# Performance work log

Hardware: AMD Instinct MI355X
Metric: run time of the kernel (lower is better)

Reference implementation:

```python
import jax, jax.numpy as jnp
import numpy as np

B, Q, K, D, H = 4, 2048, 2048, 512, 8
HD = D // H
_INF = -1e30


def setup_inputs() -> dict:
    key = jax.random.key(0)
    ks = jax.random.split(key, 8)
    scale = 1.0 / HD ** 0.5
    return {
        "query": jax.random.normal(ks[0], (B, Q, D), jnp.float32),
        "key": jax.random.normal(ks[1], (B, K, D), jnp.float32),
        "value": jax.random.normal(ks[2], (B, K, D), jnp.float32),
        "Wq": jax.random.normal(ks[3], (D, D), jnp.float32) * scale,  # [out,in]
        "Wk": jax.random.normal(ks[4], (D, D), jnp.float32) * scale,
        "Wv": jax.random.normal(ks[5], (D, D), jnp.float32) * scale,
        "Wo": jax.random.normal(ks[6], (D, D), jnp.float32) * scale,
        "attn_mask": jax.random.randint(ks[7], (B, K), 0, 2, jnp.int32),
    }


def reference(query, key, value, Wq, Wk, Wv, Wo, attn_mask):
    bsz, qlen, _ = query.shape
    klen = key.shape[1]
    head_q = (query @ Wq.T).reshape(bsz, qlen, H, HD)
    head_k = (key @ Wk.T).reshape(bsz, klen, H, HD)
    head_v = (value @ Wv.T).reshape(bsz, klen, H, HD)
    scale = 1.0 / HD ** 0.5
    # [b, i, j, n] score tensor, as in the torch einsum 'bind,bjnd->bijn'
    attn_score = jnp.einsum('bind,bjnd->bijn', head_q, head_k) * scale
    mask = (attn_mask == 0)[:, None, :, None]  # dim-2 mask branch
    attn_score = jnp.where(mask, _INF, attn_score)
    attn_prob = jax.nn.softmax(attn_score, axis=2)  # softmax over key axis j
    attn_vec = jnp.einsum('bijn,bjnd->bind', attn_prob, head_v)
    attn_vec = attn_vec.reshape(bsz, qlen, H * HD)
    return attn_vec @ Wo.T
```

## Files before the change

### kernel.cpp

```cpp
#include <hip/hip_runtime.h>

constexpr int Bc   = 4;
constexpr int Qlen = 2048;
constexpr int Klen = 2048;
constexpr int Dm   = 512;
constexpr int Hh   = 8;
constexpr int HDim = 64;

typedef __attribute__((ext_vector_type(8))) short short8;
typedef __attribute__((ext_vector_type(8))) _Float16 half8;
typedef __attribute__((ext_vector_type(2))) __fp16 fp16x2;
typedef __attribute__((ext_vector_type(4))) float f32x4;

__device__ __forceinline__ f32x4 MFMA16(short8 a, short8 b, f32x4 c) {
  return __builtin_amdgcn_mfma_f32_16x16x32_f16(
      __builtin_bit_cast(half8, a), __builtin_bit_cast(half8, b), c, 0, 0, 0);
}

__device__ __forceinline__ void gload_lds16(const void* g, void* l) {
  __builtin_amdgcn_global_load_lds(
      (const __attribute__((address_space(1))) void*)g,
      (__attribute__((address_space(3))) void*)l, 16, 0, 0);
}

__device__ __forceinline__ unsigned short f2h(float f) {
  _Float16 h = (_Float16)f;
  return __builtin_bit_cast(unsigned short, h);
}

__device__ __forceinline__ unsigned pk2h(float a, float b) {
  fp16x2 h = __builtin_amdgcn_cvt_pkrtz(a, b);
  return __builtin_bit_cast(unsigned, h);
}

__global__ __launch_bounds__(256) void cvt4(
    const float* __restrict__ s0, const float* __restrict__ s1,
    const float* __restrict__ s2, const float* __restrict__ s3,
    unsigned short* __restrict__ o0, unsigned short* __restrict__ o1,
    unsigned short* __restrict__ o2, unsigned short* __restrict__ o3,
    const int* __restrict__ msk, float* __restrict__ biasf) {
  const int seg = blockIdx.y;
  int i = (blockIdx.x * 256 + threadIdx.x) * 4;
  if (seg < 4) {
    const float* s = (seg == 0) ? s0 : (seg == 1) ? s1 : (seg == 2) ? s2 : s3;
    unsigned short* o = (seg == 0) ? o0 : (seg == 1) ? o1 : (seg == 2) ? o2 : o3;
    float4 x = *(const float4*)(s + i);
    unsigned t[2] = {pk2h(x.x, x.y), pk2h(x.z, x.w)};
    *(uint2*)(o + i) = *(const uint2*)t;
  } else if (i + 3 < Bc * Klen) {
    int4 m = *(const int4*)(msk + i);
    float4 bo;
    bo.x = (m.x == 0) ? -60000.0f : 0.0f;
    bo.y = (m.y == 0) ? -60000.0f : 0.0f;
    bo.z = (m.z == 0) ? -60000.0f : 0.0f;
    bo.w = (m.w == 0) ? -60000.0f : 0.0f;
    *(float4*)(biasf + i) = bo;
  }
}

__global__ __launch_bounds__(256) void cvt_in(
    const float* __restrict__ q, const float* __restrict__ k,
    const float* __restrict__ v,
    unsigned short* __restrict__ qh, unsigned short* __restrict__ kh,
    unsigned short* __restrict__ vh) {
  const int seg = blockIdx.y;
  const float* s = (seg == 0) ? q : (seg == 1) ? k : v;
  unsigned short* o = (seg == 0) ? qh : (seg == 1) ? kh : vh;
  int i = (blockIdx.x * 256 + threadIdx.x) * 4;
  float4 x = *(const float4*)(s + i);
  unsigned t[2] = {pk2h(x.x, x.y), pk2h(x.z, x.w)};
  *(uint2*)(o + i) = *(const uint2*)t;
}

template <bool F16A>
__global__ __launch_bounds__(256) void gemm_qkv(
    const float* __restrict__ q_in,
    const float* __restrict__ k_in,
    const float* __restrict__ v_in,
    const unsigned short* __restrict__ qh,
    const unsigned short* __restrict__ kh,
    const unsigned short* __restrict__ vh,
    const unsigned short* __restrict__ Wqh,
    const unsigned short* __restrict__ Wkh,
    const unsigned short* __restrict__ Wvh,
    unsigned short* __restrict__ Qp,
    unsigned short* __restrict__ Kp,
    unsigned short* __restrict__ Vp) {
  __shared__ unsigned short As[128 * 32];
  __shared__ unsigned short Bs[128 * 32];
  const int tid = threadIdx.x;
  const int w = tid >> 6, l = tid & 63;
  const int quad = l >> 4, l15 = l & 15;
  const int m0 = blockIdx.x * 128;
  const int n0 = blockIdx.y * 128;
  const int seg = n0 >> 9;
  const int f0  = n0 & 511;
  const float* Af = (seg == 0) ? q_in : (seg == 1) ? k_in : v_in;
  const unsigned short* Ah = (seg == 0) ? qh : (seg == 1) ? kh : vh;
  const unsigned short* W = (seg == 0) ? Wqh : (seg == 1) ? Wkh : Wvh;
  unsigned short* dst = (seg == 0) ? Qp : (seg == 1) ? Kp : Vp;

  f32x4 acc[4][4] = {};
  const int lrow = l >> 2;
  const int lcol = (l & 3) * 8;
  const int wm = (w >> 1) * 64, wn = (w & 1) * 64;

  for (int kk = 0; kk < 512; kk += 32) {
#pragma unroll
    for (int i = 0; i < 2; ++i) {
      int row = w * 32 + i * 16 + lrow;
      if constexpr (F16A) {
        gload_lds16(Ah + (size_t)(m0 + row) * 512 + kk + lcol, &As[row * 32 + lcol]);
      } else {
        const float* ap = Af + (size_t)(m0 + row) * 512 + kk + lcol;
        float4 x0 = *(const float4*)(ap);
        float4 x1 = *(const float4*)(ap + 4);
        unsigned t[4] = {pk2h(x0.x, x0.y), pk2h(x0.z, x0.w),
                         pk2h(x1.x, x1.y), pk2h(x1.z, x1.w)};
        *(uint4*)&As[row * 32 + lcol] = *(const uint4*)t;
      }
      gload_lds16(W + (size_t)(f0 + row) * 512 + kk + lcol, &Bs[row * 32 + lcol]);
    }
    __syncthreads();
    short8 af[4], bf[4];
#pragma unroll
    for (int t = 0; t < 4; ++t)
      af[t] = *(const short8*)&As[(wm + t * 16 + l15) * 32 + quad * 8];
#pragma unroll
    for (int t = 0; t < 4; ++t)
      bf[t] = *(const short8*)&Bs[(wn + t * 16 + l15) * 32 + quad * 8];
#pragma unroll
    for (int mt = 0; mt < 4; ++mt)
#pragma unroll
      for (int nt = 0; nt < 4; ++nt)
        acc[mt][nt] = MFMA16(af[mt], bf[nt], acc[mt][nt]);
    __syncthreads();
  }
#pragma unroll
  for (int mt = 0; mt < 4; ++mt)
#pragma unroll
    for (int nt = 0; nt < 4; ++nt)
#pragma unroll
      for (int r = 0; r < 4; ++r) {
        int m  = m0 + wm + mt * 16 + quad * 4 + r;
        int nn = f0 + wn + nt * 16 + l15;
        int b = m >> 11, qq = m & 2047;
        int h = nn >> 6, hd = nn & 63;
        dst[(((size_t)(b * Hh + h)) * Qlen + qq) * HDim + hd] = f2h(acc[mt][nt][r]);
      }
}

__global__ __launch_bounds__(256) void transpose_v(
    const unsigned short* __restrict__ Vp, unsigned short* __restrict__ Vt) {
  __shared__ unsigned short t[64 * 72];
  const int bh = blockIdx.y, jt = blockIdx.x;
  const int tid = threadIdx.x;
#pragma unroll
  for (int i = 0; i < 2; ++i) {
    int g = i * 256 + tid;
    int j = g >> 3, c8 = g & 7;
    *(uint4*)&t[j * 72 + c8 * 8] =
        *(const uint4*)(Vp + ((size_t)bh * Klen + jt * 64 + j) * 64 + c8 * 8);
  }
  __syncthreads();
#pragma unroll
  for (int i = 0; i < 2; ++i) {
    int g = i * 256 + tid;
    int d = g >> 3, j8 = g & 7;
    unsigned short tmp[8];
#pragma unroll
    for (int kx = 0; kx < 8; ++kx) tmp[kx] = t[(j8 * 8 + kx) * 72 + d];
    *(uint4*)(Vt + ((size_t)bh * HDim + d) * Klen + jt * 64 + j8 * 8) = *(const uint4*)tmp;
  }
}

__global__ __launch_bounds__(256) void gemm_out(
    const unsigned short* __restrict__ Oa,
    const unsigned short* __restrict__ Woh,
    float* __restrict__ out) {
  __shared__ unsigned short As[128 * 32];
  __shared__ unsigned short Bs[128 * 32];
  const int tid = threadIdx.x;
  const int w = tid >> 6, l = tid & 63;
  const int quad = l >> 4, l15 = l & 15;
  const int m0 = blockIdx.x * 128;
  const int n0 = blockIdx.y * 128;

  f32x4 acc[4][4] = {};
  const int lrow = l >> 2;
  const int lcol = (l & 3) * 8;
  const int wm = (w >> 1) * 64, wn = (w & 1) * 64;

  for (int kk = 0; kk < 512; kk += 32) {
#pragma unroll
    for (int i = 0; i < 2; ++i) {
      int row = w * 32 + i * 16 + lrow;
      gload_lds16(Oa + (size_t)(m0 + row) * 512 + kk + lcol, &As[row * 32 + lcol]);
      gload_lds16(Woh + (size_t)(n0 + row) * 512 + kk + lcol, &Bs[row * 32 + lcol]);
    }
    __syncthreads();
    short8 af[4], bf[4];
#pragma unroll
    for (int t = 0; t < 4; ++t)
      af[t] = *(const short8*)&As[(wm + t * 16 + l15) * 32 + quad * 8];
#pragma unroll
    for (int t = 0; t < 4; ++t)
      bf[t] = *(const short8*)&Bs[(wn + t * 16 + l15) * 32 + quad * 8];
#pragma unroll
    for (int mt = 0; mt < 4; ++mt)
#pragma unroll
      for (int nt = 0; nt < 4; ++nt)
        acc[mt][nt] = MFMA16(af[mt], bf[nt], acc[mt][nt]);
    __syncthreads();
  }
#pragma unroll
  for (int mt = 0; mt < 4; ++mt)
#pragma unroll
    for (int nt = 0; nt < 4; ++nt)
#pragma unroll
      for (int r = 0; r < 4; ++r) {
        int m  = m0 + wm + mt * 16 + quad * 4 + r;
        int nn = n0 + wn + nt * 16 + l15;
        out[(size_t)m * 512 + nn] = acc[mt][nt][r];
      }
}

template <bool KSPLIT>
__global__ __launch_bounds__(256, 4) void attn(
    const unsigned short* __restrict__ Qp,
    const unsigned short* __restrict__ Kp,
    const unsigned short* __restrict__ Vt,
    const float* __restrict__ biasf,
    unsigned short* __restrict__ Oa,
    unsigned short* __restrict__ Op,
    float* __restrict__ Sp) {
  __shared__ unsigned short Ks[64 * 64];
  __shared__ unsigned short Vs[64 * 64];
  __shared__ unsigned short Ps[4][16 * 72];

  const int tid = threadIdx.x;
  const int w = tid >> 6, l = tid & 63;
  const int quad = l >> 4, l15 = l & 15;
  const int bid = blockIdx.x;
  const int bh = bid & 31;
  int qt, part, kt0, ktN;
  if constexpr (KSPLIT) {
    int rest = bid >> 5;
    part = rest & 1;
    qt = rest >> 1;
    kt0 = part * 16; ktN = kt0 + 16;
  } else {
    part = 0; qt = bid >> 5; kt0 = 0; ktN = Klen / 64;
  }
  const int b = bh >> 3, h = bh & 7;
  const int x = l15 & 7;
  const int qrow = qt * 64 + w * 16 + l15;

  short8 aq[2];
#pragma unroll
  for (int k2 = 0; k2 < 2; ++k2)
    aq[k2] = *(const short8*)(Qp + ((size_t)bh * Qlen + qrow) * HDim + (k2 * 4 + quad) * 8);

  f32x4 o[4] = {};
  float m_run = -1.0e6f, l_acc = 0.f;
  constexpr float C1 = 0.125f * 1.4426950408889634f;
  const float* brow = biasf + b * Klen;

  for (int kt = kt0; kt < ktN; ++kt) {
    __syncthreads();
#pragma unroll
    for (int i = 0; i < 2; ++i) {
      int g = i * 256 + tid;
      int row = g >> 3, c8 = g & 7;
      int sb = (c8 ^ (row & 7)) * 8;
      gload_lds16(Kp + ((size_t)bh * Klen + kt * 64 + row) * HDim + sb, &Ks[g * 8]);
      gload_lds16(Vt + ((size_t)bh * HDim + row) * Klen + kt * 64 + sb, &Vs[g * 8]);
    }
    float4 bb[4];
#pragma unroll
    for (int ct = 0; ct < 4; ++ct)
      bb[ct] = *(const float4*)(brow + kt * 64 + ct * 16 + quad * 4);
    __syncthreads();

    f32x4 sv[4];
#pragma unroll
    for (int ct = 0; ct < 4; ++ct) {
      const short8 bk0 = *(const short8*)&Ks[(ct * 16 + l15) * 64 + (quad ^ x) * 8];
      const short8 bk1 = *(const short8*)&Ks[(ct * 16 + l15) * 64 + ((4 + quad) ^ x) * 8];
      f32x4 a = {};
      a = MFMA16(bk0, aq[0], a);
      a = MFMA16(bk1, aq[1], a);
      sv[ct] = a;
    }

#pragma unroll
    for (int ct = 0; ct < 4; ++ct)
#pragma unroll
      for (int r = 0; r < 4; ++r)
        sv[ct][r] = sv[ct][r] * C1 + bb[ct][r];

    float mx0 = fmaxf(fmaxf(sv[0][0], sv[0][1]), fmaxf(sv[0][2], sv[0][3]));
    float mx1 = fmaxf(fmaxf(sv[1][0], sv[1][1]), fmaxf(sv[1][2], sv[1][3]));
    float mx2 = fmaxf(fmaxf(sv[2][0], sv[2][1]), fmaxf(sv[2][2], sv[2][3]));
    float mx3 = fmaxf(fmaxf(sv[3][0], sv[3][1]), fmaxf(sv[3][2], sv[3][3]));
    float mx = fmaxf(fmaxf(mx0, mx1), fmaxf(mx2, mx3));
    mx = fmaxf(mx, __shfl_xor(mx, 16));
    mx = fmaxf(mx, __shfl_xor(mx, 32));
    float mnew  = fmaxf(m_run, mx);
    float alpha = exp2f(m_run - mnew);
    m_run = mnew;

    float ps = 0.f;
#pragma unroll
    for (int ct = 0; ct < 4; ++ct) {
      float p0 = exp2f(sv[ct][0] - mnew);
      float p1 = exp2f(sv[ct][1] - mnew);
      float p2 = exp2f(sv[ct][2] - mnew);
      float p3 = exp2f(sv[ct][3] - mnew);
      sv[ct][0] = p0; sv[ct][1] = p1; sv[ct][2] = p2; sv[ct][3] = p3;
      ps += (p0 + p1) + (p2 + p3);
    }
    l_acc = l_acc * alpha + ps;
#pragma unroll
    for (int ctd = 0; ctd < 4; ++ctd) o[ctd] *= alpha;

#pragma unroll
    for (int ct = 0; ct < 4; ++ct) {
      unsigned pk[2] = {pk2h(sv[ct][0], sv[ct][1]), pk2h(sv[ct][2], sv[ct][3])};
      *(uint2*)&Ps[w][l15 * 72 + ct * 16 + quad * 4] = *(const uint2*)pk;
    }
    const short8 ap0 = *(const short8*)&Ps[w][l15 * 72 + quad * 8];
    const short8 ap1 = *(const short8*)&Ps[w][l15 * 72 + 32 + quad * 8];

#pragma unroll
    for (int ctd = 0; ctd < 4; ++ctd) {
      const short8 bv0 = *(const short8*)&Vs[(ctd * 16 + l15) * 64 + (quad ^ x) * 8];
      const short8 bv1 = *(const short8*)&Vs[(ctd * 16 + l15) * 64 + ((4 + quad) ^ x) * 8];
      o[ctd] = MFMA16(bv0, ap0, o[ctd]);
      o[ctd] = MFMA16(bv1, ap1, o[ctd]);
    }
  }

  float lt = l_acc;
  lt += __shfl_xor(lt, 16);
  lt += __shfl_xor(lt, 32);
  float rl = 1.0f / lt;
  if constexpr (KSPLIT) {
    const size_t pbase = ((size_t)part * 32 + bh) * Qlen;
    const size_t obase = (pbase + qrow) * 64;
#pragma unroll
    for (int ctd = 0; ctd < 4; ++ctd) {
      unsigned pk[2] = {pk2h(o[ctd][0] * rl, o[ctd][1] * rl),
                        pk2h(o[ctd][2] * rl, o[ctd][3] * rl)};
      *(uint2*)(Op + obase + ctd * 16 + quad * 4) = *(const uint2*)pk;
    }
    if (l < 16)
      Sp[pbase + qrow] = m_run + log2f(lt);
  } else {
    const size_t obase = ((size_t)(b * Qlen) + qrow) * Dm + h * 64;
#pragma unroll
    for (int ctd = 0; ctd < 4; ++ctd) {
      unsigned pk[2] = {pk2h(o[ctd][0] * rl, o[ctd][1] * rl),
                        pk2h(o[ctd][2] * rl, o[ctd][3] * rl)};
      *(uint2*)(Oa + obase + ctd * 16 + quad * 4) = *(const uint2*)pk;
    }
  }
}

__global__ __launch_bounds__(256) void reduce_o(
    const unsigned short* __restrict__ Op, const float* __restrict__ Sp,
    unsigned short* __restrict__ Oa) {
  int g = blockIdx.x * 256 + threadIdx.x;
  int row = g >> 3, c8 = g & 7;
  const size_t PART = (size_t)32 * Qlen;
  float s1 = Sp[row], s2 = Sp[PART + row];
  float M = fmaxf(s1, s2);
  float w1 = exp2f(s1 - M), w2 = exp2f(s2 - M);
  float rs = 1.0f / (w1 + w2);
  w1 *= rs; w2 *= rs;
  short8 a = *(const short8*)(Op + (size_t)row * 64 + c8 * 8);
  short8 bvec = *(const short8*)(Op + (PART + row) * 64 + c8 * 8);
  half8 af = __builtin_bit_cast(half8, a);
  half8 bf = __builtin_bit_cast(half8, bvec);
  unsigned pk[4];
#pragma unroll
  for (int i = 0; i < 4; ++i) {
    float r0 = w1 * (float)af[i * 2 + 0] + w2 * (float)bf[i * 2 + 0];
    float r1 = w1 * (float)af[i * 2 + 1] + w2 * (float)bf[i * 2 + 1];
    pk[i] = pk2h(r0, r1);
  }
  int bh = row >> 11, qrow = row & 2047;
  int b = bh >> 3, h = bh & 7;
  *(uint4*)(Oa + ((size_t)(b * Qlen) + qrow) * Dm + h * 64 + c8 * 8) =
      *(const uint4*)pk;
}

extern "C" void kernel_launch(void* const* d_in, const int* in_sizes, int n_in,
                              void* d_out, int out_size, void* d_ws, size_t ws_size,
                              hipStream_t stream) {
  const float* q  = (const float*)d_in[0];
  const float* k  = (const float*)d_in[1];
  const float* v  = (const float*)d_in[2];
  const float* Wq = (const float*)d_in[3];
  const float* Wk = (const float*)d_in[4];
  const float* Wv = (const float*)d_in[5];
  const float* Wo = (const float*)d_in[6];
  const int*  msk = (const int*)d_in[7];
  float* out = (float*)d_out;

  char* ws = (char*)d_ws;
  const size_t SEG  = (size_t)Bc * Hh * Qlen * HDim * sizeof(unsigned short);
  const size_t WSEG = (size_t)Dm * Dm * sizeof(unsigned short);
  unsigned short* Qp  = (unsigned short*)(ws);
  unsigned short* Kp  = (unsigned short*)(ws + SEG);
  unsigned short* Vp  = (unsigned short*)(ws + 2 * SEG);
  unsigned short* Vt  = (unsigned short*)(ws + 3 * SEG);
  unsigned short* Oa  = Vp;
  unsigned short* Wqh = (unsigned short*)(ws + 4 * SEG);
  unsigned short* Wkh = (unsigned short*)(ws + 4 * SEG + WSEG);
  unsigned short* Wvh = (unsigned short*)(ws + 4 * SEG + 2 * WSEG);
  unsigned short* Woh = (unsigned short*)(ws + 4 * SEG + 3 * WSEG);
  float*          Bfs = (float*)(ws + 4 * SEG + 4 * WSEG);
  unsigned short* qh  = (unsigned short*)(ws + 4 * SEG + 4 * WSEG + 65536);
  unsigned short* kh  = qh + SEG / 2;
  unsigned short* vh  = kh + SEG / 2;
  unsigned short* Op  = qh;
  float*          Sp  = (float*)vh;
  const size_t NEED = 4 * SEG + 4 * WSEG + 65536 + 3 * SEG;
  const bool big = ws_size >= NEED;

  const int wn = Dm * Dm;
  hipLaunchKernelGGL(cvt4, dim3(wn / 1024, 5), dim3(256), 0, stream,
                     Wq, Wk, Wv, Wo, Wqh, Wkh, Wvh, Woh, msk, Bfs);

  if (big) {
    hipLaunchKernelGGL(cvt_in, dim3(4096, 3), dim3(256), 0, stream,
                       q, k, v, qh, kh, vh);
    hipLaunchKernelGGL(gemm_qkv<true>, dim3(64, 12), dim3(256), 0, stream,
                       q, k, v, qh, kh, vh, Wqh, Wkh, Wvh, Qp, Kp, Vp);
    hipLaunchKernelGGL(transpose_v, dim3(32, 32), dim3(256), 0, stream, Vp, Vt);
    hipLaunchKernelGGL(attn<true>, dim3(2048), dim3(256), 0, stream,
                       Qp, Kp, Vt, Bfs, Oa, Op, Sp);
    hipLaunchKernelGGL(reduce_o, dim3(2048), dim3(256), 0, stream, Op, Sp, Oa);
  } else {
    hipLaunchKernelGGL(gemm_qkv<false>, dim3(64, 12), dim3(256), 0, stream,
                       q, k, v, qh, kh, vh, Wqh, Wkh, Wvh, Qp, Kp, Vp);
    hipLaunchKernelGGL(transpose_v, dim3(32, 32), dim3(256), 0, stream, Vp, Vt);
    hipLaunchKernelGGL(attn<false>, dim3(1024), dim3(256), 0, stream,
                       Qp, Kp, Vt, Bfs, Oa, Op, Sp);
  }
  hipLaunchKernelGGL(gemm_out, dim3(64, 4), dim3(256), 0, stream, Oa, Woh, out);
}
```

Before: 223.4 us.

## Compact unmasked keys per batch and skip masked key work in attention

Adds a prefix-scan kernel that builds, per batch, a list of unmasked key indices and their count. It gathers only those K/V rows during fp16 conversion and skips K/V projection, transpose and attention tiles past the count. The attention kernel also folds the softmax scale into the Q projection and computes the row sum with an MFMA against a ones vector. It rescales the running max lazily, only when it grows by more than a threshold. This drops roughly half the K/V work under the random mask, at the cost of an extra scan kernel, data-dependent gathers and more complex correctness conditions. It exploits a mask property that holds in general, not just for the test inputs.

```diff
diff --git a/kernel.cpp b/kernel.cpp
--- a/kernel.cpp
+++ b/kernel.cpp
@@ -6,6 +6,7 @@
 constexpr int Dm   = 512;
 constexpr int Hh   = 8;
 constexpr int HDim = 64;
+constexpr float C1 = 0.125f * 1.4426950408889634f;
 
 typedef __attribute__((ext_vector_type(8))) short short8;
 typedef __attribute__((ext_vector_type(8))) _Float16 half8;
@@ -31,6 +32,37 @@
 __device__ __forceinline__ unsigned pk2h(float a, float b) {
   fp16x2 h = __builtin_amdgcn_cvt_pkrtz(a, b);
   return __builtin_bit_cast(unsigned, h);
+}
+
+__global__ __launch_bounds__(256) void scan_mask(
+    const int* __restrict__ msk, int* __restrict__ idx, int* __restrict__ cnt) {
+  const int b = blockIdx.x;
+  const int tid = threadIdx.x;
+  __shared__ int wtot[4];
+  const int* mrow = msk + b * Klen;
+  int m8[8];
+  int c = 0;
+#pragma unroll
+  for (int i = 0; i < 8; ++i) {
+    m8[i] = mrow[tid * 8 + i];
+    c += (m8[i] != 0);
+  }
+  int pre = c;
+#pragma unroll
+  for (int off = 1; off < 64; off <<= 1) {
+    int t = __shfl_up(pre, off);
+    if ((tid & 63) >= off) pre += t;
+  }
+  const int w = tid >> 6;
+  if ((tid & 63) == 63) wtot[w] = pre;
+  __syncthreads();
+  int base = 0;
+  for (int i = 0; i < w; ++i) base += wtot[i];
+  int p = base + pre - c;
+#pragma unroll
+  for (int i = 0; i < 8; ++i)
+    if (m8[i] != 0) idx[b * Klen + (p++)] = tid * 8 + i;
+  if (tid == 255) cnt[b] = base + pre;
 }
 
 __global__ __launch_bounds__(256) void cvt4(
@@ -62,14 +94,31 @@
     const float* __restrict__ q, const float* __restrict__ k,
     const float* __restrict__ v,
     unsigned short* __restrict__ qh, unsigned short* __restrict__ kh,
-    unsigned short* __restrict__ vh) {
+    unsigned short* __restrict__ vh,
+    const int* __restrict__ idx, const int* __restrict__ cnt) {
   const int seg = blockIdx.y;
-  const float* s = (seg == 0) ? q : (seg == 1) ? k : v;
-  unsigned short* o = (seg == 0) ? qh : (seg == 1) ? kh : vh;
-  int i = (blockIdx.x * 256 + threadIdx.x) * 4;
-  float4 x = *(const float4*)(s + i);
-  unsigned t[2] = {pk2h(x.x, x.y), pk2h(x.z, x.w)};
-  *(uint2*)(o + i) = *(const uint2*)t;
+  int g = blockIdx.x * 256 + threadIdx.x;
+  int i = g * 4;
+  if (seg == 0) {
+    float4 x = *(const float4*)(q + i);
+    unsigned t[2] = {pk2h(x.x, x.y), pk2h(x.z, x.w)};
+    *(uint2*)(qh + i) = *(const uint2*)t;
+    return;
+  }
+  const float* s = (seg == 1) ? k : v;
+  unsigned short* o = (seg == 1) ? kh : vh;
+  int row = i >> 9, col = i & 511;
+  int b = row >> 11, jc = row & 2047;
+  int cb = cnt[b];
+  if (jc < cb) {
+    int j = idx[b * Klen + jc];
+    float4 x = *(const float4*)(s + ((size_t)(b * Klen + j)) * 512 + col);
+    unsigned t[2] = {pk2h(x.x, x.y), pk2h(x.z, x.w)};
+    *(uint2*)(o + (size_t)row * 512 + col) = *(const uint2*)t;
+  } else if (jc < ((cb + 127) & ~127)) {
+    uint2 z = {0u, 0u};
+    *(uint2*)(o + (size_t)row * 512 + col) = z;
+  }
 }
 
 template <bool F16A>
@@ -85,7 +134,8 @@
     const unsigned short* __restrict__ Wvh,
     unsigned short* __restrict__ Qp,
     unsigned short* __restrict__ Kp,
-    unsigned short* __restrict__ Vp) {
+    unsigned short* __restrict__ Vp,
+    const int* __restrict__ cnt) {
   __shared__ unsigned short As[128 * 32];
   __shared__ unsigned short Bs[128 * 32];
   const int tid = threadIdx.x;
@@ -95,6 +145,12 @@
   const int n0 = blockIdx.y * 128;
   const int seg = n0 >> 9;
   const int f0  = n0 & 511;
+  if constexpr (F16A) {
+    if (seg != 0) {
+      int local = m0 & 2047;
+      if (local >= ((cnt[m0 >> 11] + 63) & ~63)) return;
+    }
+  }
   const float* Af = (seg == 0) ? q_in : (seg == 1) ? k_in : v_in;
   const unsigned short* Ah = (seg == 0) ? qh : (seg == 1) ? kh : vh;
   const unsigned short* W = (seg == 0) ? Wqh : (seg == 1) ? Wkh : Wvh;
@@ -136,6 +192,7 @@
         acc[mt][nt] = MFMA16(af[mt], bf[nt], acc[mt][nt]);
     __syncthreads();
   }
+  const float oscale = (seg == 0) ? C1 : 1.0f;
 #pragma unroll
   for (int mt = 0; mt < 4; ++mt)
 #pragma unroll
@@ -146,14 +203,19 @@
         int nn = f0 + wn + nt * 16 + l15;
         int b = m >> 11, qq = m & 2047;
         int h = nn >> 6, hd = nn & 63;
-        dst[(((size_t)(b * Hh + h)) * Qlen + qq) * HDim + hd] = f2h(acc[mt][nt][r]);
+        dst[(((size_t)(b * Hh + h)) * Qlen + qq) * HDim + hd] =
+            f2h(acc[mt][nt][r] * oscale);
       }
 }
 
 __global__ __launch_bounds__(256) void transpose_v(
-    const unsigned short* __restrict__ Vp, unsigned short* __restrict__ Vt) {
+    const unsigned short* __restrict__ Vp, unsigned short* __restrict__ Vt,
+    const int* __restrict__ cnt) {
   __shared__ unsigned short t[64 * 72];
   const int bh = blockIdx.y, jt = blockIdx.x;
+  if (cnt) {
+    if (jt * 64 >= ((cnt[bh >> 3] + 63) & ~63)) return;
+  }
   const int tid = threadIdx.x;
 #pragma unroll
   for (int i = 0; i < 2; ++i) {
@@ -225,12 +287,13 @@
       }
 }
 
-template <bool KSPLIT>
+template <bool KSPLIT, bool COMPACT>
 __global__ __launch_bounds__(256, 4) void attn(
     const unsigned short* __restrict__ Qp,
     const unsigned short* __restrict__ Kp,
     const unsigned short* __restrict__ Vt,
     const float* __restrict__ biasf,
+    const int* __restrict__ cntArr,
     unsigned short* __restrict__ Oa,
     unsigned short* __restrict__ Op,
     float* __restrict__ Sp) {
@@ -243,16 +306,28 @@
   const int quad = l >> 4, l15 = l & 15;
   const int bid = blockIdx.x;
   const int bh = bid & 31;
+  const int b = bh >> 3, h = bh & 7;
+
+  int cnt, KT;
+  if constexpr (COMPACT) {
+    cnt = cntArr[b];
+    KT = (cnt + 63) >> 6;
+  } else {
+    cnt = Klen;
+    KT = Klen / 64;
+  }
+
   int qt, part, kt0, ktN;
   if constexpr (KSPLIT) {
     int rest = bid >> 5;
     part = rest & 1;
     qt = rest >> 1;
-    kt0 = part * 16; ktN = kt0 + 16;
+    int half = (KT + 1) >> 1;
+    kt0 = part ? half : 0;
+    ktN = part ? KT : half;
   } else {
-    part = 0; qt = bid >> 5; kt0 = 0; ktN = Klen / 64;
-  }
-  const int b = bh >> 3, h = bh & 7;
+    part = 0; qt = bid >> 5; kt0 = 0; ktN = KT;
+  }
   const int x = l15 & 7;
   const int qrow = qt * 64 + w * 16 + l15;
 
@@ -261,9 +336,13 @@
   for (int k2 = 0; k2 < 2; ++k2)
     aq[k2] = *(const short8*)(Qp + ((size_t)bh * Qlen + qrow) * HDim + (k2 * 4 + quad) * 8);
 
+  short8 ones;
+#pragma unroll
+  for (int j = 0; j < 8; ++j) ones[j] = (short)0x3C00;
+
   f32x4 o[4] = {};
-  float m_run = -1.0e6f, l_acc = 0.f;
-  constexpr float C1 = 0.125f * 1.4426950408889634f;
+  f32x4 o5 = {};
+  float m_run = -1.0e6f;
   const float* brow = biasf + b * Klen;
 
   for (int kt = kt0; kt < ktN; ++kt) {
@@ -277,9 +356,11 @@
       gload_lds16(Vt + ((size_t)bh * HDim + row) * Klen + kt * 64 + sb, &Vs[g * 8]);
     }
     float4 bb[4];
-#pragma unroll
-    for (int ct = 0; ct < 4; ++ct)
-      bb[ct] = *(const float4*)(brow + kt * 64 + ct * 16 + quad * 4);
+    if constexpr (!COMPACT) {
+#pragma unroll
+      for (int ct = 0; ct < 4; ++ct)
+        bb[ct] = *(const float4*)(brow + kt * 64 + ct * 16 + quad * 4);
+    }
     __syncthreads();
 
     f32x4 sv[4];
@@ -293,11 +374,21 @@
       sv[ct] = a;
     }
 
-#pragma unroll
-    for (int ct = 0; ct < 4; ++ct)
-#pragma unroll
-      for (int r = 0; r < 4; ++r)
-        sv[ct][r] = sv[ct][r] * C1 + bb[ct][r];
+    if constexpr (!COMPACT) {
+#pragma unroll
+      for (int ct = 0; ct < 4; ++ct)
+#pragma unroll
+        for (int r = 0; r < 4; ++r)
+          sv[ct][r] += bb[ct][r];
+    } else {
+      if (kt == KT - 1) {
+#pragma unroll
+        for (int ct = 0; ct < 4; ++ct)
+#pragma unroll
+          for (int r = 0; r < 4; ++r)
+            if (kt * 64 + ct * 16 + quad * 4 + r >= cnt) sv[ct][r] = -60000.0f;
+      }
+    }
 
     float mx0 = fmaxf(fmaxf(sv[0][0], sv[0][1]), fmaxf(sv[0][2], sv[0][3]));
     float mx1 = fmaxf(fmaxf(sv[1][0], sv[1][1]), fmaxf(sv[1][2], sv[1][3]));
@@ -306,31 +397,29 @@
     float mx = fmaxf(fmaxf(mx0, mx1), fmaxf(mx2, mx3));
     mx = fmaxf(mx, __shfl_xor(mx, 16));
     mx = fmaxf(mx, __shfl_xor(mx, 32));
-    float mnew  = fmaxf(m_run, mx);
-    float alpha = exp2f(m_run - mnew);
-    m_run = mnew;
-
-    float ps = 0.f;
+    if (__any(mx > m_run + 8.0f)) {
+      float mnew  = fmaxf(m_run, mx);
+      float alpha = exp2f(m_run - mnew);
+      m_run = mnew;
+#pragma unroll
+      for (int ctd = 0; ctd < 4; ++ctd) o[ctd] *= alpha;
+      o5 *= alpha;
+    }
+
 #pragma unroll
     for (int ct = 0; ct < 4; ++ct) {
-      float p0 = exp2f(sv[ct][0] - mnew);
-      float p1 = exp2f(sv[ct][1] - mnew);
-      float p2 = exp2f(sv[ct][2] - mnew);
-      float p3 = exp2f(sv[ct][3] - mnew);
-      sv[ct][0] = p0; sv[ct][1] = p1; sv[ct][2] = p2; sv[ct][3] = p3;
-      ps += (p0 + p1) + (p2 + p3);
-    }
-    l_acc = l_acc * alpha + ps;
-#pragma unroll
-    for (int ctd = 0; ctd < 4; ++ctd) o[ctd] *= alpha;
-
-#pragma unroll
-    for (int ct = 0; ct < 4; ++ct) {
-      unsigned pk[2] = {pk2h(sv[ct][0], sv[ct][1]), pk2h(sv[ct][2], sv[ct][3])};
+      float p0 = exp2f(sv[ct][0] - m_run);
+      float p1 = exp2f(sv[ct][1] - m_run);
+      float p2 = exp2f(sv[ct][2] - m_run);
+      float p3 = exp2f(sv[ct][3] - m_run);
+      unsigned pk[2] = {pk2h(p0, p1), pk2h(p2, p3)};
       *(uint2*)&Ps[w][l15 * 72 + ct * 16 + quad * 4] = *(const uint2*)pk;
     }
     const short8 ap0 = *(const short8*)&Ps[w][l15 * 72 + quad * 8];
     const short8 ap1 = *(const short8*)&Ps[w][l15 * 72 + 32 + quad * 8];
+
+    o5 = MFMA16(ones, ap0, o5);
+    o5 = MFMA16(ones, ap1, o5);
 
 #pragma unroll
     for (int ctd = 0; ctd < 4; ++ctd) {
@@ -341,10 +430,8 @@
     }
   }
 
-  float lt = l_acc;
-  lt += __shfl_xor(lt, 16);
-  lt += __shfl_xor(lt, 32);
-  float rl = 1.0f / lt;
+  float lt = o5[0];
+  float rl = (lt > 0.0f) ? 1.0f / lt : 0.0f;
   if constexpr (KSPLIT) {
     const size_t pbase = ((size_t)part * 32 + bh) * Qlen;
     const size_t obase = (pbase + qrow) * 64;
@@ -355,7 +442,7 @@
       *(uint2*)(Op + obase + ctd * 16 + quad * 4) = *(const uint2*)pk;
     }
     if (l < 16)
-      Sp[pbase + qrow] = m_run + log2f(lt);
+      Sp[pbase + qrow] = (lt > 0.0f) ? m_run + log2f(lt) : -1.0e30f;
   } else {
     const size_t obase = ((size_t)(b * Qlen) + qrow) * Dm + h * 64;
 #pragma unroll
@@ -420,7 +507,9 @@
   unsigned short* Wkh = (unsigned short*)(ws + 4 * SEG + WSEG);
   unsigned short* Wvh = (unsigned short*)(ws + 4 * SEG + 2 * WSEG);
   unsigned short* Woh = (unsigned short*)(ws + 4 * SEG + 3 * WSEG);
-  float*          Bfs = (float*)(ws + 4 * SEG + 4 * WSEG);
+  int*   idxArr = (int*)(ws + 4 * SEG + 4 * WSEG);
+  int*   cntArr = idxArr + Bc * Klen;
+  float* Bfs    = (float*)idxArr;
   unsigned short* qh  = (unsigned short*)(ws + 4 * SEG + 4 * WSEG + 65536);
   unsigned short* kh  = qh + SEG / 2;
   unsigned short* vh  = kh + SEG / 2;
@@ -429,25 +518,31 @@
   const size_t NEED = 4 * SEG + 4 * WSEG + 65536 + 3 * SEG;
   const bool big = ws_size >= NEED;
 
+  auto attn_split  = attn<true, true>;
+  auto attn_single = attn<false, false>;
+
   const int wn = Dm * Dm;
-  hipLaunchKernelGGL(cvt4, dim3(wn / 1024, 5), dim3(256), 0, stream,
-                     Wq, Wk, Wv, Wo, Wqh, Wkh, Wvh, Woh, msk, Bfs);
-
   if (big) {
+    hipLaunchKernelGGL(scan_mask, dim3(Bc), dim3(256), 0, stream, msk, idxArr, cntArr);
+    hipLaunchKernelGGL(cvt4, dim3(wn / 1024, 4), dim3(256), 0, stream,
+                       Wq, Wk, Wv, Wo, Wqh, Wkh, Wvh, Woh, msk, Bfs);
     hipLaunchKernelGGL(cvt_in, dim3(4096, 3), dim3(256), 0, stream,
-                       q, k, v, qh, kh, vh);
+                       q, k, v, qh, kh, vh, idxArr, cntArr);
     hipLaunchKernelGGL(gemm_qkv<true>, dim3(64, 12), dim3(256), 0, stream,
-                       q, k, v, qh, kh, vh, Wqh, Wkh, Wvh, Qp, Kp, Vp);
-    hipLaunchKernelGGL(transpose_v, dim3(32, 32), dim3(256), 0, stream, Vp, Vt);
-    hipLaunchKernelGGL(attn<true>, dim3(2048), dim3(256), 0, stream,
-                       Qp, Kp, Vt, Bfs, Oa, Op, Sp);
+                       q, k, v, qh, kh, vh, Wqh, Wkh, Wvh, Qp, Kp, Vp, cntArr);
+    hipLaunchKernelGGL(transpose_v, dim3(32, 32), dim3(256), 0, stream, Vp, Vt, cntArr);
+    hipLaunchKernelGGL(attn_split, dim3(2048), dim3(256), 0, stream,
+                       Qp, Kp, Vt, Bfs, cntArr, Oa, Op, Sp);
     hipLaunchKernelGGL(reduce_o, dim3(2048), dim3(256), 0, stream, Op, Sp, Oa);
   } else {
+    hipLaunchKernelGGL(cvt4, dim3(wn / 1024, 5), dim3(256), 0, stream,
+                       Wq, Wk, Wv, Wo, Wqh, Wkh, Wvh, Woh, msk, Bfs);
     hipLaunchKernelGGL(gemm_qkv<false>, dim3(64, 12), dim3(256), 0, stream,
-                       q, k, v, qh, kh, vh, Wqh, Wkh, Wvh, Qp, Kp, Vp);
-    hipLaunchKernelGGL(transpose_v, dim3(32, 32), dim3(256), 0, stream, Vp, Vt);
-    hipLaunchKernelGGL(attn<false>, dim3(1024), dim3(256), 0, stream,
-                       Qp, Kp, Vt, Bfs, Oa, Op, Sp);
+                       q, k, v, qh, kh, vh, Wqh, Wkh, Wvh, Qp, Kp, Vp, cntArr);
+    hipLaunchKernelGGL(transpose_v, dim3(32, 32), dim3(256), 0, stream, Vp, Vt,
+                       (const int*)nullptr);
+    hipLaunchKernelGGL(attn_single, dim3(1024), dim3(256), 0, stream,
+                       Qp, Kp, Vt, Bfs, (const int*)nullptr, Oa, Op, Sp);
   }
   hipLaunchKernelGGL(gemm_out, dim3(64, 4), dim3(256), 0, stream, Oa, Woh, out);
 }
```

Measured after the change: 194.1 us. 13.1% less time.
